# Optimization experiments

Measured on AMD Instinct MI355X. Metric: run time of the kernel, lower is better.

## Reference

```python
import jax, jax.numpy as jnp
import numpy as np


def setup_inputs() -> dict:
    key = jax.random.key(0)
    k1, k2, k3 = jax.random.split(key, 3)
    B, T, D = 2, 2048, 1024
    x = jax.random.normal(k1, (B, T, D), dtype=jnp.float32)
    w_qkv = jax.random.normal(k2, (3 * D, D), dtype=jnp.float32) * (D ** -0.5)
    w_out = jax.random.normal(k3, (D, D), dtype=jnp.float32) * (D ** -0.5)
    return {"x": x, "w_qkv": w_qkv, "w_out": w_out, "heads": 16}


def reference(x, w_qkv, w_out, heads):
    # SelfAttention forward: attention_type='sdp', position_mode='alibi', causal=True, eval mode.
    B, T, D = x.shape
    H = heads
    hd = D // H
    scale = hd ** -0.5

    # qkv projection: torch Linear -> x @ W^T
    qkv = (x @ w_qkv.T).reshape(B, T, 3, H, hd)
    qkv = jnp.transpose(qkv, (2, 0, 3, 1, 4))  # [3, B, H, T, hd]
    q, k, v = qkv[0], qkv[1], qkv[2]

    # ALiBi relative bias: slopes = 1 / 2^(h/H) for h = 1..H
    slopes = 1.0 / jnp.power(2.0, jnp.arange(1, H + 1, dtype=jnp.float32) / H)
    pos = jnp.arange(T, dtype=jnp.float32)
    rel = jnp.abs(pos[:, None] - pos[None, :])  # [T, T]
    bias = -slopes[None, :, None, None] * rel[None, None, :, :]  # [1, H, T, T]

    # scores + causal mask + softmax (manual path since position_bias is not None)
    scores = jnp.einsum('bhqd,bhkd->bhqk', q, k) * scale + bias
    causal_mask = jnp.triu(jnp.ones((T, T), dtype=bool), k=1)
    scores = jnp.where(causal_mask[None, None, :, :], -jnp.inf, scores)
    attn = jax.nn.softmax(scores, axis=-1)
    attn = jnp.where(jnp.isnan(attn), 1.0 / float(max(T, 1)), attn)

    out = jnp.einsum('bhqk,bhkd->bhqd', attn, v)  # [B, H, T, hd]
    out = jnp.transpose(out, (0, 2, 1, 3)).reshape(B, T, D)
    return out @ w_out.T
```

## Files before the change

kernel.cpp:

```cpp
#include <hip/hip_runtime.h>
#include <hip/hip_bf16.h>

typedef __attribute__((ext_vector_type(8))) short shortx8;
typedef __attribute__((ext_vector_type(4))) float floatx4;
typedef __attribute__((ext_vector_type(4))) unsigned uintx4;
typedef __attribute__((ext_vector_type(2))) unsigned uintx2;

#define B_ 2
#define T_ 2048
#define D_ 1024
#define H_ 16
#define HD_ 64
#define SCALE 0.125f
#define SMAX 16.0f
#define FULLH ((size_t)B_ * H_ * T_ * HD_)

#define GLDS16(g, l) __builtin_amdgcn_global_load_lds( \
    (__attribute__((address_space(1))) void*)(g), \
    (__attribute__((address_space(3))) void*)(l), 16, 0, 0)

__device__ __forceinline__ short f2bf(float f) {
    union { float f; unsigned u; } v; v.f = f;
    unsigned r = v.u + 0x7FFFu + ((v.u >> 16) & 1u);
    return (short)(r >> 16);
}

__device__ __forceinline__ unsigned pk2(float x, float y) {
    union { __hip_bfloat162 h; unsigned u; } t;
    t.h = __float22bfloat162_rn(make_float2(x, y));
    return t.u;
}

__device__ __forceinline__ shortx8 cvt8(floatx4 a, floatx4 b) {
    uintx4 r = { pk2(a[0], a[1]), pk2(a[2], a[3]), pk2(b[0], b[1]), pk2(b[2], b[3]) };
    return __builtin_bit_cast(shortx8, r);
}

__global__ __launch_bounds__(256) void cvt_bf(const float* __restrict__ src,
                                              short* __restrict__ dst, int n8) {
    int i = blockIdx.x * 256 + threadIdx.x;
    if (i < n8) {
        const floatx4* p = reinterpret_cast<const floatx4*>(src) + (size_t)i * 2;
        *(reinterpret_cast<shortx8*>(dst) + i) = cvt8(p[0], p[1]);
    }
}


__global__ __launch_bounds__(256) void qkv_fast(const short* __restrict__ xbf,
                                                const short* __restrict__ wbf,
                                                short* __restrict__ qout,
                                                short* __restrict__ kv) {
    __shared__ __align__(16) short As[128 * 64];
    __shared__ __align__(16) short Bs[128 * 64];

    const int tid = threadIdx.x;
    const int wv = tid >> 6;
    const int l  = tid & 63;
    const int ln = l & 15;
    const int quad = l >> 4;
    const int rowb = quad << 2;
    const int wm = wv >> 1, wn = wv & 1;
    const int m0 = blockIdx.y * 128;
    const int n0g = blockIdx.x * 128;

    const int lr = l >> 3, lc = l & 7;
    const int gcol = (lc ^ lr) << 3;
    const short* agp = xbf + (size_t)(m0 + wv * 32 + lr) * D_ + gcol;
    const short* bgp = wbf + (size_t)(n0g + wv * 32 + lr) * D_ + gcol;
    short* aldsb = As + wv * 32 * 64;
    short* bldsb = Bs + wv * 32 * 64;

    floatx4 acc[4][4] = {};

    for (int k0 = 0; k0 < D_; k0 += 64) {
        __syncthreads();
#pragma unroll
        for (int c = 0; c < 4; ++c) {
            GLDS16(agp + (size_t)(c * 8) * D_ + k0, aldsb + c * 512);
            GLDS16(bgp + (size_t)(c * 8) * D_ + k0, bldsb + c * 512);
        }
        __syncthreads();

#pragma unroll
        for (int kk = 0; kk < 2; ++kk) {
            const int csw = (kk << 2) + quad;
            const int sw = (csw ^ (ln & 7)) << 3;
            shortx8 af[4], bf[4];
#pragma unroll
            for (int i = 0; i < 4; ++i)
                af[i] = *reinterpret_cast<const shortx8*>(&As[((wm * 64 + i * 16 + ln) << 6) + sw]);
#pragma unroll
            for (int j = 0; j < 4; ++j)
                bf[j] = *reinterpret_cast<const shortx8*>(&Bs[((wn * 64 + j * 16 + ln) << 6) + sw]);
#pragma unroll
            for (int i = 0; i < 4; ++i)
#pragma unroll
                for (int j = 0; j < 4; ++j)
                    acc[i][j] = __builtin_amdgcn_mfma_f32_16x16x32_bf16(af[i], bf[j], acc[i][j], 0, 0, 0);
        }
    }

    const int sel = n0g >> 10;
    const int bb = m0 >> 11;
    const int t0w = (m0 + wm * 64) & (T_ - 1);
    const int h = ((n0g + wn * 64) >> 6) & 15;

    if (sel < 2) {
        short* dst = (sel == 0) ? qout : kv;
        const float sc = (sel == 0) ? SCALE : 1.0f;
        const size_t hb = (size_t)(bb * H_ + h) * T_;
#pragma unroll
        for (int i = 0; i < 4; ++i)
#pragma unroll
            for (int r = 0; r < 4; ++r) {
                int t = t0w + i * 16 + rowb + r;
#pragma unroll
                for (int j = 0; j < 4; ++j)
                    dst[(hb + t) * HD_ + j * 16 + ln] = f2bf(acc[i][j][r] * sc);
            }
    } else {
        __syncthreads();
        short* tb = (wv < 2) ? (As + wv * 4096) : (Bs + (wv - 2) * 4096);
        short* vhead = kv + FULLH + (size_t)(bb * H_ + h) * HD_ * T_;
        const int dl = l & 31, th = (l >> 5) << 5;
#pragma unroll
        for (int p = 0; p < 2; ++p) {
#pragma unroll
            for (int i = 0; i < 4; ++i)
#pragma unroll
                for (int jj = 0; jj < 2; ++jj) {
                    int j = 2 * p + jj;
#pragma unroll
                    for (int r = 0; r < 4; ++r)
                        tb[(jj * 16 + ln) * 72 + i * 16 + rowb + r] = f2bf(acc[i][j][r]);
                }
            short* vd = vhead + (size_t)(p * 32 + dl) * T_ + t0w + th;
#pragma unroll
            for (int seg = 0; seg < 4; ++seg)
                *reinterpret_cast<shortx8*>(vd + seg * 8) =
                    *reinterpret_cast<const shortx8*>(&tb[dl * 72 + th + seg * 8]);
        }
    }
}

__global__ __launch_bounds__(256) void out_fast(const short* __restrict__ Abf,
                                                const short* __restrict__ wbf,
                                                float* __restrict__ out) {
    __shared__ __align__(16) short As[128 * 64];
    __shared__ __align__(16) short Bs[128 * 64];

    const int tid = threadIdx.x;
    const int wv = tid >> 6;
    const int l  = tid & 63;
    const int ln = l & 15;
    const int quad = l >> 4;
    const int rowb = quad << 2;
    const int wm = wv >> 1, wn = wv & 1;
    const int m0 = blockIdx.y * 128;
    const int n0g = blockIdx.x * 128;

    const int lr = l >> 3, lc = l & 7;
    const int gcol = (lc ^ lr) << 3;
    const short* bgp = wbf + (size_t)(n0g + wv * 32 + lr) * D_ + gcol;
    short* aldsb = As + wv * 32 * 64;
    short* bldsb = Bs + wv * 32 * 64;

    size_t abase[4];
#pragma unroll
    for (int c = 0; c < 4; ++c) {
        int m = m0 + wv * 32 + c * 8 + lr;
        int bb2 = m >> 11, t = m & (T_ - 1);
        abase[c] = ((size_t)(bb2 * H_) * T_ + t) * HD_ + gcol;
    }

    floatx4 acc[4][4] = {};

    for (int k0 = 0; k0 < D_; k0 += 64) {
        const size_t hoff = (size_t)(k0 >> 6) * T_ * HD_;
        __syncthreads();
#pragma unroll
        for (int c = 0; c < 4; ++c) {
            GLDS16(Abf + abase[c] + hoff, aldsb + c * 512);
            GLDS16(bgp + (size_t)(c * 8) * D_ + k0, bldsb + c * 512);
        }
        __syncthreads();

#pragma unroll
        for (int kk = 0; kk < 2; ++kk) {
            const int csw = (kk << 2) + quad;
            const int sw = (csw ^ (ln & 7)) << 3;
            shortx8 af[4], bf[4];
#pragma unroll
            for (int i = 0; i < 4; ++i)
                af[i] = *reinterpret_cast<const shortx8*>(&As[((wm * 64 + i * 16 + ln) << 6) + sw]);
#pragma unroll
            for (int j = 0; j < 4; ++j)
                bf[j] = *reinterpret_cast<const shortx8*>(&Bs[((wn * 64 + j * 16 + ln) << 6) + sw]);
#pragma unroll
            for (int i = 0; i < 4; ++i)
#pragma unroll
                for (int j = 0; j < 4; ++j)
                    acc[i][j] = __builtin_amdgcn_mfma_f32_16x16x32_bf16(af[i], bf[j], acc[i][j], 0, 0, 0);
        }
    }

#pragma unroll
    for (int i = 0; i < 4; ++i)
#pragma unroll
        for (int r = 0; r < 4; ++r) {
            int m = m0 + wm * 64 + i * 16 + rowb + r;
#pragma unroll
            for (int j = 0; j < 4; ++j)
                out[(size_t)m * D_ + n0g + wn * 64 + j * 16 + ln] = acc[i][j][r];
        }
}

__global__ __launch_bounds__(256, 4) void attn(const short* __restrict__ qws,
                                               const short* __restrict__ kv,
                                               short* ao) {
    __shared__ __align__(16) short Ks[64][72];
    __shared__ __align__(16) short Vt[64][72];
    __shared__ __align__(16) short Pt[4][64][20];

    const int tid = threadIdx.x;
    const int wv   = tid >> 6;
    const int l    = tid & 63;
    const int ln   = l & 15;
    const int quad = l >> 4;
    const int qd   = quad << 3;
    const int rowb = quad << 2;

    const int xcd  = blockIdx.x & 7;
    const int slot = blockIdx.x >> 3;
    const int bh   = xcd * 4 + (slot & 3);
    const int qb   = 31 - (slot >> 2);
    const int h    = bh & 15;
    const int b    = bh >> 4;

    const float slope = exp2f(-(float)(h + 1) * (1.0f / 16.0f));
    const size_t koff = (size_t)(b * H_ + h) * T_ * HD_;
    const int q0 = qb * 64 + wv * 16;

    shortx8 qf[2];
#pragma unroll
    for (int kk = 0; kk < 2; ++kk)
        qf[kk] = *reinterpret_cast<const shortx8*>(&qws[koff + (size_t)(q0 + ln) * HD_ + kk * 32 + qd]);

    const int r0 = tid >> 3, c0 = (tid & 7) << 3, r1 = r0 + 32;
    const short* kbase = kv + koff;
    const short* vbase = kv + FULLH + koff;
    shortx8 kA, kB, vA, vB;
    auto FETCH = [&](int kb) {
        const short* kp = kbase + ((size_t)(kb * 64) << 6);
        kA = *reinterpret_cast<const shortx8*>(kp + ((size_t)r0 << 6) + c0);
        kB = *reinterpret_cast<const shortx8*>(kp + ((size_t)r1 << 6) + c0);
        const short* vp = vbase + kb * 64;
        vA = *reinterpret_cast<const shortx8*>(vp + ((size_t)r0 << 11) + c0);
        vB = *reinterpret_cast<const shortx8*>(vp + ((size_t)r1 << 11) + c0);
    };

    floatx4 oacc[4] = {};
    floatx4 lsum = {};
    const shortx8 ones = {16256, 16256, 16256, 16256, 16256, 16256, 16256, 16256};
    const float base0 = -SMAX - slope * (float)(q0 + rowb);

    FETCH(0);
    for (int kb = 0; kb <= qb; ++kb) {
        __syncthreads();
        *reinterpret_cast<shortx8*>(&Ks[r0][c0]) = kA;
        *reinterpret_cast<shortx8*>(&Ks[r1][c0]) = kB;
        *reinterpret_cast<shortx8*>(&Vt[r0][c0]) = vA;
        *reinterpret_cast<shortx8*>(&Vt[r1][c0]) = vB;
        __syncthreads();
        if (kb < qb) FETCH(kb + 1);

        const bool diag = (kb == qb);
        const int ncmax = diag ? (wv + 1) : 4;
        const int kln = kb * 64 + ln;
        const float bb0 = slope * (float)kln + base0;

#pragma unroll
        for (int nc = 0; nc < 4; ++nc) {
            floatx4 s = {};
            if (nc < ncmax) {
#pragma unroll
                for (int kk = 0; kk < 2; ++kk) {
                    shortx8 bfr = *reinterpret_cast<const shortx8*>(&Ks[nc * 16 + ln][kk * 32 + qd]);
                    s = __builtin_amdgcn_mfma_f32_16x16x32_bf16(qf[kk], bfr, s, 0, 0, 0);
                }
            }
            float p[4];
#pragma unroll
            for (int r = 0; r < 4; ++r) {
                bool ok = (kln + nc * 16) <= (q0 + rowb + r);
                float e = __expf(s[r] + bb0 + slope * (float)(nc * 16 - r));
                p[r] = ok ? e : 0.0f;
            }
            uintx2 pkd = { pk2(p[0], p[1]), pk2(p[2], p[3]) };
            *reinterpret_cast<uintx2*>(&Pt[wv][nc * 16 + ln][rowb]) = pkd;
        }

#pragma unroll
        for (int kk = 0; kk < 2; ++kk) {
            if (diag && kk * 32 > wv * 16 + 15) continue;
            shortx8 pf;
#pragma unroll
            for (int j = 0; j < 8; ++j) pf[j] = Pt[wv][kk * 32 + qd + j][ln];
            lsum = __builtin_amdgcn_mfma_f32_16x16x32_bf16(pf, ones, lsum, 0, 0, 0);
#pragma unroll
            for (int nc = 0; nc < 4; ++nc) {
                shortx8 bfr = *reinterpret_cast<const shortx8*>(&Vt[nc * 16 + ln][kk * 32 + qd]);
                oacc[nc] = __builtin_amdgcn_mfma_f32_16x16x32_bf16(pf, bfr, oacc[nc], 0, 0, 0);
            }
        }
    }

#pragma unroll
    for (int r = 0; r < 4; ++r) {
        float inv = 1.0f / lsum[r];
        int t = q0 + rowb + r;
#pragma unroll
        for (int nc = 0; nc < 4; ++nc)
            ao[koff + (size_t)t * HD_ + nc * 16 + ln] = f2bf(oacc[nc][r] * inv);
    }
}

__global__ __launch_bounds__(256) void qkv_slow(const float* __restrict__ x,
                                                const float* __restrict__ wqkv,
                                                short* __restrict__ qout,
                                                short* __restrict__ kv) {
    __shared__ __align__(16) short As[64][72];
    __shared__ __align__(16) short Bs[64][72];
    const int tid = threadIdx.x;
    const int wv = tid >> 6, l = tid & 63, ln = l & 15, quad = l >> 4, qd = quad << 3;
    const int m0 = blockIdx.y * 64;
    const int sel = blockIdx.x >> 4, h = blockIdx.x & 15;
    const int nrow = sel * D_ + h * HD_;
    const int sr0 = tid >> 3, sc0 = (tid & 7) << 3, sr1 = sr0 + 32;
    floatx4 fa[4], fb[4];
    auto FETCH = [&](int k0) {
        const float* ap = &x[(size_t)(m0 + sr0) * D_ + k0 + sc0];
        fa[0] = *reinterpret_cast<const floatx4*>(ap);
        fa[1] = *reinterpret_cast<const floatx4*>(ap + 4);
        ap += (size_t)32 * D_;
        fa[2] = *reinterpret_cast<const floatx4*>(ap);
        fa[3] = *reinterpret_cast<const floatx4*>(ap + 4);
        const float* bp = &wqkv[(size_t)(nrow + sr0) * D_ + k0 + sc0];
        fb[0] = *reinterpret_cast<const floatx4*>(bp);
        fb[1] = *reinterpret_cast<const floatx4*>(bp + 4);
        bp += (size_t)32 * D_;
        fb[2] = *reinterpret_cast<const floatx4*>(bp);
        fb[3] = *reinterpret_cast<const floatx4*>(bp + 4);
    };
    floatx4 acc[4] = {};
    FETCH(0);
    for (int k0 = 0; k0 < D_; k0 += 64) {
        __syncthreads();
        *reinterpret_cast<shortx8*>(&As[sr0][sc0]) = cvt8(fa[0], fa[1]);
        *reinterpret_cast<shortx8*>(&As[sr1][sc0]) = cvt8(fa[2], fa[3]);
        *reinterpret_cast<shortx8*>(&Bs[sr0][sc0]) = cvt8(fb[0], fb[1]);
        *reinterpret_cast<shortx8*>(&Bs[sr1][sc0]) = cvt8(fb[2], fb[3]);
        __syncthreads();
        if (k0 + 64 < D_) FETCH(k0 + 64);
        const int mr = (wv << 4) + ln;
#pragma unroll
        for (int kk = 0; kk < 2; ++kk) {
            shortx8 a = *reinterpret_cast<const shortx8*>(&As[mr][kk * 32 + qd]);
#pragma unroll
            for (int nc = 0; nc < 4; ++nc) {
                shortx8 b = *reinterpret_cast<const shortx8*>(&Bs[nc * 16 + ln][kk * 32 + qd]);
                acc[nc] = __builtin_amdgcn_mfma_f32_16x16x32_bf16(a, b, acc[nc], 0, 0, 0);
            }
        }
    }
    const int bb = m0 >> 11, t0 = m0 & (T_ - 1);
    if (sel < 2) {
        short* dst = (sel == 0) ? qout : kv;
        const float sc = (sel == 0) ? SCALE : 1.0f;
#pragma unroll
        for (int r = 0; r < 4; ++r) {
            int t = t0 + (wv << 4) + (quad << 2) + r;
#pragma unroll
            for (int nc = 0; nc < 4; ++nc)
                dst[((size_t)(bb * H_ + h) * T_ + t) * HD_ + nc * 16 + ln] = f2bf(acc[nc][r] * sc);
        }
    } else {
        __syncthreads();
#pragma unroll
        for (int r = 0; r < 4; ++r)
#pragma unroll
            for (int nc = 0; nc < 4; ++nc)
                As[nc * 16 + ln][(wv << 4) + (quad << 2) + r] = f2bf(acc[nc][r]);
        __syncthreads();
        const int d = tid >> 2, tseg = (tid & 3) << 4;
        short* vdst = kv + FULLH + ((size_t)(bb * H_ + h) * HD_ + d) * T_ + t0 + tseg;
        *reinterpret_cast<shortx8*>(vdst)     = *reinterpret_cast<const shortx8*>(&As[d][tseg]);
        *reinterpret_cast<shortx8*>(vdst + 8) = *reinterpret_cast<const shortx8*>(&As[d][tseg + 8]);
    }
}

__global__ __launch_bounds__(256) void out_slow(const short* __restrict__ A,
                                                const float* __restrict__ W,
                                                float* __restrict__ out) {
    __shared__ __align__(16) short As[64][72];
    __shared__ __align__(16) short Bs[64][72];
    const int tid = threadIdx.x;
    const int wv = tid >> 6, l = tid & 63, ln = l & 15, quad = l >> 4, qd = quad << 3;
    const int m0 = blockIdx.y * 64, n0 = blockIdx.x * 64;
    const int sr0 = tid >> 3, sc0 = (tid & 7) << 3, sr1 = sr0 + 32;
    shortx8 sa0, sa1;
    floatx4 fb[4];
    auto FETCH = [&](int k0) {
        const int h = k0 >> 6;
        int m = m0 + sr0;
        int bb = m >> 11, t = m & (T_ - 1);
        sa0 = *reinterpret_cast<const shortx8*>(A + ((size_t)(bb * H_ + h) * T_ + t) * HD_ + sc0);
        m = m0 + sr1; bb = m >> 11; t = m & (T_ - 1);
        sa1 = *reinterpret_cast<const shortx8*>(A + ((size_t)(bb * H_ + h) * T_ + t) * HD_ + sc0);
        const float* bp = &W[(size_t)(n0 + sr0) * D_ + k0 + sc0];
        fb[0] = *reinterpret_cast<const floatx4*>(bp);
        fb[1] = *reinterpret_cast<const floatx4*>(bp + 4);
        bp += (size_t)32 * D_;
        fb[2] = *reinterpret_cast<const floatx4*>(bp);
        fb[3] = *reinterpret_cast<const floatx4*>(bp + 4);
    };
    floatx4 acc[4] = {};
    FETCH(0);
    for (int k0 = 0; k0 < D_; k0 += 64) {
        __syncthreads();
        *reinterpret_cast<shortx8*>(&As[sr0][sc0]) = sa0;
        *reinterpret_cast<shortx8*>(&As[sr1][sc0]) = sa1;
        *reinterpret_cast<shortx8*>(&Bs[sr0][sc0]) = cvt8(fb[0], fb[1]);
        *reinterpret_cast<shortx8*>(&Bs[sr1][sc0]) = cvt8(fb[2], fb[3]);
        __syncthreads();
        if (k0 + 64 < D_) FETCH(k0 + 64);
        const int mr = (wv << 4) + ln;
#pragma unroll
        for (int kk = 0; kk < 2; ++kk) {
            shortx8 a = *reinterpret_cast<const shortx8*>(&As[mr][kk * 32 + qd]);
#pragma unroll
            for (int nc = 0; nc < 4; ++nc) {
                shortx8 b = *reinterpret_cast<const shortx8*>(&Bs[nc * 16 + ln][kk * 32 + qd]);
                acc[nc] = __builtin_amdgcn_mfma_f32_16x16x32_bf16(a, b, acc[nc], 0, 0, 0);
            }
        }
    }
#pragma unroll
    for (int r = 0; r < 4; ++r) {
        int m = m0 + (wv << 4) + (quad << 2) + r;
#pragma unroll
        for (int nc = 0; nc < 4; ++nc)
            out[(size_t)m * D_ + n0 + nc * 16 + ln] = acc[nc][r];
    }
}

extern "C" void kernel_launch(void* const* d_in, const int* in_sizes, int n_in,
                              void* d_out, int out_size, void* d_ws, size_t ws_size,
                              hipStream_t stream) {
    const float* x    = (const float*)d_in[0];
    const float* wqkv = (const float*)d_in[1];
    const float* wout = (const float*)d_in[2];

    short* kvbuf = (short*)d_out;
    float* out   = (float*)d_out;

    if (ws_size >= 23068672ULL) {
        short* xbf  = (short*)d_ws;
        short* wbf  = xbf + 4 * 1024 * 1024;
        short* qws  = xbf + 7 * 1024 * 1024;
        short* wobf = xbf;

        cvt_bf<<<2048, 256, 0, stream>>>(x, xbf, 524288);
        cvt_bf<<<1536, 256, 0, stream>>>(wqkv, wbf, 393216);
        qkv_fast<<<dim3(24, 32), 256, 0, stream>>>(xbf, wbf, qws, kvbuf);
        cvt_bf<<<512, 256, 0, stream>>>(wout, wobf, 131072);
        attn<<<dim3(1024), 256, 0, stream>>>(qws, kvbuf, qws);
        out_fast<<<dim3(8, 32), 256, 0, stream>>>(qws, wobf, out);
    } else {
        short* qws = (short*)d_ws;
        qkv_slow<<<dim3(48, 64), 256, 0, stream>>>(x, wqkv, qws, kvbuf);
        attn<<<dim3(1024), 256, 0, stream>>>(qws, kvbuf, qws);
        out_slow<<<dim3(16, 64), 256, 0, stream>>>(qws, wout, out);
    }
}
```

Measured before the change: 191.7 us.

## Fuse conversion launches, use exp2 softmax, split diagonal path, add setprio

Merges the x and w_qkv bf16 conversions into one launch and folds the w_out conversion into extra blocks of the attention kernel, which removes two launches. Q is pre-scaled by log2(e) so the softmax can use the hardware exp2 instruction, and the per-column ALiBi offsets are precomputed into registers. The attention inner loop gets a mask-free path for off-diagonal blocks, the P tile row padding changes, and the PV MFMA section is wrapped in s_setprio. The extra conversion blocks in the attention grid could compete with attention work, and the changed LDS padding may alter bank conflicts.

```diff
diff --git a/kernel.cpp b/kernel.cpp
--- a/kernel.cpp
+++ b/kernel.cpp
@@ -12,7 +12,8 @@
 #define H_ 16
 #define HD_ 64
 #define SCALE 0.125f
-#define SMAX 16.0f
+#define QSCALE 0.18033688011112042f
+#define SMAX2 23.083120654223414f
 #define FULLH ((size_t)B_ * H_ * T_ * HD_)
 
 #define GLDS16(g, l) __builtin_amdgcn_global_load_lds( \
@@ -36,13 +37,24 @@
     return __builtin_bit_cast(shortx8, r);
 }
 
-__global__ __launch_bounds__(256) void cvt_bf(const float* __restrict__ src,
-                                              short* __restrict__ dst, int n8) {
+__device__ __forceinline__ float ex2(float x) {
+#if __has_builtin(__builtin_amdgcn_exp2f)
+    return __builtin_amdgcn_exp2f(x);
+#else
+    return exp2f(x);
+#endif
+}
+
+__global__ __launch_bounds__(256) void cvt_xw(const float* __restrict__ x,
+                                              const float* __restrict__ wqkv,
+                                              short* __restrict__ xbf,
+                                              short* __restrict__ wbf) {
     int i = blockIdx.x * 256 + threadIdx.x;
-    if (i < n8) {
-        const floatx4* p = reinterpret_cast<const floatx4*>(src) + (size_t)i * 2;
-        *(reinterpret_cast<shortx8*>(dst) + i) = cvt8(p[0], p[1]);
-    }
+    const float* src; short* dst; int o;
+    if (i < 524288) { src = x; dst = xbf; o = i; }
+    else            { src = wqkv; dst = wbf; o = i - 524288; }
+    const floatx4* p = reinterpret_cast<const floatx4*>(src) + (size_t)o * 2;
+    *(reinterpret_cast<shortx8*>(dst) + o) = cvt8(p[0], p[1]);
 }
 
 
@@ -107,7 +119,7 @@
 
     if (sel < 2) {
         short* dst = (sel == 0) ? qout : kv;
-        const float sc = (sel == 0) ? SCALE : 1.0f;
+        const float sc = (sel == 0) ? QSCALE : 1.0f;
         const size_t hb = (size_t)(bb * H_ + h) * T_;
 #pragma unroll
         for (int i = 0; i < 4; ++i)
@@ -217,10 +229,19 @@
 
 __global__ __launch_bounds__(256, 4) void attn(const short* __restrict__ qws,
                                                const short* __restrict__ kv,
-                                               short* ao) {
+                                               short* ao,
+                                               const float* __restrict__ wout,
+                                               short* __restrict__ wobf) {
+    if (blockIdx.x >= 1024) {
+        int i = (blockIdx.x - 1024) * 256 + threadIdx.x;
+        const floatx4* p = reinterpret_cast<const floatx4*>(wout) + (size_t)i * 2;
+        *(reinterpret_cast<shortx8*>(wobf) + i) = cvt8(p[0], p[1]);
+        return;
+    }
+
     __shared__ __align__(16) short Ks[64][72];
     __shared__ __align__(16) short Vt[64][72];
-    __shared__ __align__(16) short Pt[4][64][20];
+    __shared__ __align__(16) short Pt[4][64][18];
 
     const int tid = threadIdx.x;
     const int wv   = tid >> 6;
@@ -237,7 +258,7 @@
     const int h    = bh & 15;
     const int b    = bh >> 4;
 
-    const float slope = exp2f(-(float)(h + 1) * (1.0f / 16.0f));
+    const float slope2 = 1.4426950408889634f * exp2f(-(float)(h + 1) * 0.0625f);
     const size_t koff = (size_t)(b * H_ + h) * T_ * HD_;
     const int q0 = qb * 64 + wv * 16;
 
@@ -262,7 +283,14 @@
     floatx4 oacc[4] = {};
     floatx4 lsum = {};
     const shortx8 ones = {16256, 16256, 16256, 16256, 16256, 16256, 16256, 16256};
-    const float base0 = -SMAX - slope * (float)(q0 + rowb);
+    const float base0 = -SMAX2 - slope2 * (float)(q0 + rowb);
+
+    float sncr[4][4];
+#pragma unroll
+    for (int nc = 0; nc < 4; ++nc)
+#pragma unroll
+        for (int r = 0; r < 4; ++r)
+            sncr[nc][r] = slope2 * (float)(nc * 16 - r);
 
     FETCH(0);
     for (int kb = 0; kb <= qb; ++kb) {
@@ -275,31 +303,54 @@
         if (kb < qb) FETCH(kb + 1);
 
         const bool diag = (kb == qb);
-        const int ncmax = diag ? (wv + 1) : 4;
         const int kln = kb * 64 + ln;
-        const float bb0 = slope * (float)kln + base0;
-
-#pragma unroll
-        for (int nc = 0; nc < 4; ++nc) {
-            floatx4 s = {};
-            if (nc < ncmax) {
+        const float bb0 = slope2 * (float)kln + base0;
+
+        if (!diag) {
+#pragma unroll
+            for (int nc = 0; nc < 4; ++nc) {
+                floatx4 s = {};
 #pragma unroll
                 for (int kk = 0; kk < 2; ++kk) {
                     shortx8 bfr = *reinterpret_cast<const shortx8*>(&Ks[nc * 16 + ln][kk * 32 + qd]);
                     s = __builtin_amdgcn_mfma_f32_16x16x32_bf16(qf[kk], bfr, s, 0, 0, 0);
                 }
+                unsigned w0 = pk2(ex2(s[0] + (bb0 + sncr[nc][0])),
+                                  ex2(s[1] + (bb0 + sncr[nc][1])));
+                unsigned w1 = pk2(ex2(s[2] + (bb0 + sncr[nc][2])),
+                                  ex2(s[3] + (bb0 + sncr[nc][3])));
+                short* pp = &Pt[wv][nc * 16 + ln][rowb];
+                *reinterpret_cast<unsigned*>(pp) = w0;
+                *reinterpret_cast<unsigned*>(pp + 2) = w1;
             }
-            float p[4];
-#pragma unroll
-            for (int r = 0; r < 4; ++r) {
-                bool ok = (kln + nc * 16) <= (q0 + rowb + r);
-                float e = __expf(s[r] + bb0 + slope * (float)(nc * 16 - r));
-                p[r] = ok ? e : 0.0f;
+        } else {
+            const int ncmax = wv + 1;
+#pragma unroll
+            for (int nc = 0; nc < 4; ++nc) {
+                floatx4 s = {};
+                if (nc < ncmax) {
+#pragma unroll
+                    for (int kk = 0; kk < 2; ++kk) {
+                        shortx8 bfr = *reinterpret_cast<const shortx8*>(&Ks[nc * 16 + ln][kk * 32 + qd]);
+                        s = __builtin_amdgcn_mfma_f32_16x16x32_bf16(qf[kk], bfr, s, 0, 0, 0);
+                    }
+                }
+                float p[4];
+#pragma unroll
+                for (int r = 0; r < 4; ++r) {
+                    bool ok = (kln + nc * 16) <= (q0 + rowb + r);
+                    float e = ex2(s[r] + (bb0 + sncr[nc][r]));
+                    p[r] = ok ? e : 0.0f;
+                }
+                unsigned w0 = pk2(p[0], p[1]);
+                unsigned w1 = pk2(p[2], p[3]);
+                short* pp = &Pt[wv][nc * 16 + ln][rowb];
+                *reinterpret_cast<unsigned*>(pp) = w0;
+                *reinterpret_cast<unsigned*>(pp + 2) = w1;
             }
-            uintx2 pkd = { pk2(p[0], p[1]), pk2(p[2], p[3]) };
-            *reinterpret_cast<uintx2*>(&Pt[wv][nc * 16 + ln][rowb]) = pkd;
-        }
-
+        }
+
+        __builtin_amdgcn_s_setprio(1);
 #pragma unroll
         for (int kk = 0; kk < 2; ++kk) {
             if (diag && kk * 32 > wv * 16 + 15) continue;
@@ -313,6 +364,7 @@
                 oacc[nc] = __builtin_amdgcn_mfma_f32_16x16x32_bf16(pf, bfr, oacc[nc], 0, 0, 0);
             }
         }
+        __builtin_amdgcn_s_setprio(0);
     }
 
 #pragma unroll
@@ -376,7 +428,7 @@
     const int bb = m0 >> 11, t0 = m0 & (T_ - 1);
     if (sel < 2) {
         short* dst = (sel == 0) ? qout : kv;
-        const float sc = (sel == 0) ? SCALE : 1.0f;
+        const float sc = (sel == 0) ? QSCALE : 1.0f;
 #pragma unroll
         for (int r = 0; r < 4; ++r) {
             int t = t0 + (wv << 4) + (quad << 2) + r;
@@ -470,16 +522,14 @@
         short* qws  = xbf + 7 * 1024 * 1024;
         short* wobf = xbf;
 
-        cvt_bf<<<2048, 256, 0, stream>>>(x, xbf, 524288);
-        cvt_bf<<<1536, 256, 0, stream>>>(wqkv, wbf, 393216);
+        cvt_xw<<<3584, 256, 0, stream>>>(x, wqkv, xbf, wbf);
         qkv_fast<<<dim3(24, 32), 256, 0, stream>>>(xbf, wbf, qws, kvbuf);
-        cvt_bf<<<512, 256, 0, stream>>>(wout, wobf, 131072);
-        attn<<<dim3(1024), 256, 0, stream>>>(qws, kvbuf, qws);
+        attn<<<dim3(1536), 256, 0, stream>>>(qws, kvbuf, qws, wout, wobf);
         out_fast<<<dim3(8, 32), 256, 0, stream>>>(qws, wobf, out);
     } else {
         short* qws = (short*)d_ws;
         qkv_slow<<<dim3(48, 64), 256, 0, stream>>>(x, wqkv, qws, kvbuf);
-        attn<<<dim3(1024), 256, 0, stream>>>(qws, kvbuf, qws);
+        attn<<<dim3(1024), 256, 0, stream>>>(qws, kvbuf, qws, nullptr, nullptr);
         out_slow<<<dim3(16, 64), 256, 0, stream>>>(qws, wout, out);
     }
 }
```

Result: faster. 184.9 us (-3.6%).
